# Kernel tuning notes

Hardware: AMD Instinct MI355X
Metric: run time of the kernel (lower is better)

Reference implementation:

```python
import jax, jax.numpy as jnp
import numpy as np

B, K, N, M = 32, 128, 128, 256  # batch, num_classes(==n_dim), n_dim, samples-per-matrix
EPSILON = 0.1
LAMBDA_SOFTMAX = 0.1
LEARNING_RATE = 0.01
BN_EPS = 1e-5


def setup_inputs() -> dict:
    key = jax.random.key(0)
    k1, k2, k3 = jax.random.split(key, 3)
    x = jax.random.normal(k1, (B, N, M), dtype=jnp.float32)
    A = jax.random.normal(k2, (K, N, N), dtype=jnp.float32) * 0.1
    EC_proto = jnp.einsum('kij,klj->kil', A, A)  # per-class PSD prototype covariances (K,N,N)
    EC_count = jax.random.uniform(k3, (K,), dtype=jnp.float32, minval=1.0, maxval=100.0)
    return {"x": x, "EC_proto": EC_proto, "EC_count": EC_count}


def reference(x, EC_proto, EC_count):
    n = x.shape[1]
    dtype = x.dtype
    # BatchNorm1d(num_classes, affine=False, track_running_stats=False): batch stats over (N, L)
    mean = x.mean(axis=(0, 2), keepdims=True)
    var = x.var(axis=(0, 2), keepdims=True)  # biased variance, as torch uses for normalization
    x = (x - mean) / jnp.sqrt(var + BN_EPS)

    eye = jnp.eye(n, dtype=dtype)
    total = EC_count.sum()
    has_counts = total > 1e-6

    # E branch: global expansion operator
    e_alpha = jnp.where(has_counts, n / (EPSILON * EPSILON * total), jnp.zeros((), dtype))
    e = e_alpha * jnp.linalg.inv(e_alpha * EC_proto.sum(0) + eye)  # (N,N)
    e_x_z = jnp.einsum('ij,bjm->bim', e, x)  # (B,N,M)

    # C branch: per-class compression operators
    bool_depth = (EC_count != 0).astype(dtype)  # (K,)
    count_fix = EC_count + (1.0 - bool_depth)
    c_alpha = (n / (count_fix * EPSILON * EPSILON) * bool_depth)[:, None, None]  # (K,1,1)
    c = c_alpha * jnp.linalg.inv(c_alpha * EC_proto + eye[None])  # (K,N,N)
    c_x_z = jnp.einsum('kij,bjm->bkim', c, x)  # (B,K,N,M)

    # Frobenius norm per (b,k), rescaled to sum to 10 over classes
    norm = jnp.sqrt((c_x_z * c_x_z).sum(axis=(2, 3)))  # (B,K)
    norm = 10.0 * norm / norm.sum(axis=1, keepdims=True)

    pi = jax.nn.softmax(-LAMBDA_SOFTMAX * norm, axis=1) * bool_depth  # (B,K)
    gama = jnp.where(has_counts, EC_count / total, jnp.zeros_like(EC_count))  # (K,)

    z_d = e_x_z - jnp.einsum('k,bkim,bk->bim', gama, c_x_z, pi)  # (B,N,M)
    return x + LEARNING_RATE * z_d
```

## Files before the change

### kernel.cpp

```cpp
#include <hip/hip_runtime.h>
#include <math.h>

#define Bb 32
#define Kk 128
#define Nn 128
#define Mm 256
#define EPS2 0.01f
#define LAMBDA_S 0.1f
#define LR 0.01f
#define BN_EPS_C 1e-5f

#define SWZ(c) (((c) & 14) | (((c) & 1) << 4) | (((c) >> 4) & 1))

__device__ __forceinline__ float readlane_f(float v, int lane) {
  return __int_as_float(__builtin_amdgcn_readlane(__float_as_int(v), lane));
}

__global__ void kA_bn_psum(const float* __restrict__ x, const float* __restrict__ P,
                           float* __restrict__ xn, float* __restrict__ Psum) {
  int t = threadIdx.x;
  if (blockIdx.x < 128) {
    int n = blockIdx.x;
    float v[32];
    float s = 0.f, s2 = 0.f;
    #pragma unroll
    for (int b = 0; b < Bb; ++b) {
      v[b] = x[(size_t)b * (Nn * Mm) + n * Mm + t];
      s += v[b];
      s2 += v[b] * v[b];
    }
    #pragma unroll
    for (int o = 32; o > 0; o >>= 1) {
      s += __shfl_down(s, o, 64);
      s2 += __shfl_down(s2, o, 64);
    }
    __shared__ float rs[4], rs2[4];
    if ((t & 63) == 0) { rs[t >> 6] = s; rs2[t >> 6] = s2; }
    __syncthreads();
    float S = rs[0] + rs[1] + rs[2] + rs[3];
    float S2 = rs2[0] + rs2[1] + rs2[2] + rs2[3];
    float mean = S * (1.0f / (Bb * Mm));
    float var = S2 * (1.0f / (Bb * Mm)) - mean * mean;
    float rstd = 1.0f / sqrtf(var + BN_EPS_C);
    #pragma unroll
    for (int b = 0; b < Bb; ++b)
      xn[(size_t)b * (Nn * Mm) + n * Mm + t] = (v[b] - mean) * rstd;
  } else {
    int e = (blockIdx.x - 128) * 256 + t;
    float s = 0.f;
    #pragma unroll 8
    for (int k = 0; k < Kk; ++k) s += P[(size_t)k * 16384 + e];
    Psum[e] = s;
  }
}

__global__ __launch_bounds__(256, 1) void k3S(
    const float* __restrict__ P, const float* __restrict__ Psum,
    const float* __restrict__ cnt, float* __restrict__ C,
    const float* __restrict__ xn, float* __restrict__ S) {
  __shared__ __align__(16) float LB[8448];
  int bx = blockIdx.x;
  int t = threadIdx.x;

  if (bx < 129) {
    float* Mt = LB;
    float* Rb = LB + 2112;
    float* redc = LB + 4160;
    int blk = bx;
    int tx = t & 15, ty = t >> 4;

    float cv = cnt[t & 127];
    float sr = cv;
    #pragma unroll
    for (int o = 32; o > 0; o >>= 1) sr += __shfl_down(sr, o, 64);
    if ((t & 63) == 0) redc[t >> 6] = sr;
    __syncthreads();
    float total = redc[0] + redc[1];
    bool has = total > 1e-6f;
    float av;
    if (blk < 128) {
      float c = cnt[blk];
      float bk = (c != 0.0f) ? 1.0f : 0.0f;
      float cfix = c + (1.0f - bk);
      av = (float)Nn / (cfix * EPS2) * bk;
    } else {
      av = has ? ((float)Nn / (EPS2 * total)) : 0.0f;
    }
    const float* src = (blk < 128) ? (P + (size_t)blk * 16384) : Psum;

    float a[8][8];
    #pragma unroll
    for (int i = 0; i < 8; ++i) {
      int row = ty * 8 + i;
      float4 p0 = *(const float4*)&src[row * 128 + tx * 8];
      float4 p1 = *(const float4*)&src[row * 128 + tx * 8 + 4];
      a[i][0] = av * p0.x; a[i][1] = av * p0.y; a[i][2] = av * p0.z; a[i][3] = av * p0.w;
      a[i][4] = av * p1.x; a[i][5] = av * p1.y; a[i][6] = av * p1.z; a[i][7] = av * p1.w;
      if (tx == ty) a[i][i] += 1.0f;
    }

    for (int kb = 0; kb < 8; ++kb) {
      int k0 = kb * 16;
      if ((ty >> 1) == kb) {
        int d = ty & 1;
        #pragma unroll
        for (int i = 0; i < 8; ++i) {
          *(float4*)&Rb[(d * 8 + i) * 128 + SWZ(2 * tx) * 4] =
              make_float4(a[i][0], a[i][1], a[i][2], a[i][3]);
          *(float4*)&Rb[(d * 8 + i) * 128 + SWZ(2 * tx + 1) * 4] =
              make_float4(a[i][4], a[i][5], a[i][6], a[i][7]);
        }
      }
      if ((tx >> 1) == kb) {
        int dh = tx & 1;
        #pragma unroll
        for (int i = 0; i < 8; ++i)
          #pragma unroll
          for (int j = 0; j < 8; ++j)
            Mt[(dh * 8 + j) * 132 + ty * 8 + i] = a[i][j];
      }
      __syncthreads();

      if (t < 64) {
        int l = t;
        float m[2][16];
        #pragma unroll
        for (int d = 0; d < 2; ++d)
          #pragma unroll
          for (int j = 0; j < 16; ++j)
            m[d][j] = Mt[j * 132 + 2 * l + d];
        #pragma unroll
        for (int q = 0; q < 16; ++q) {
          int lq = (k0 + q) >> 1;
          float pr[16];
          #pragma unroll
          for (int j = 0; j < 16; ++j) pr[j] = readlane_f(m[q & 1][j], lq);
          float piv = pr[q];
          float r0 = __builtin_amdgcn_rcpf(piv);
          float pinv = r0 * (2.0f - piv * r0);
          #pragma unroll
          for (int d = 0; d < 2; ++d) {
            float f = m[d][q];
            bool isp = (2 * l + d == k0 + q);
            float g = isp ? (1.0f - pinv) : f * pinv;
            #pragma unroll
            for (int j = 0; j < 16; ++j) m[d][j] = fmaf(-g, pr[j], m[d][j]);
            m[d][q] = isp ? pinv : -g;
          }
        }
        #pragma unroll
        for (int d = 0; d < 2; ++d)
          #pragma unroll
          for (int j = 0; j < 16; ++j)
            Mt[j * 132 + 2 * l + d] = m[d][j];
      }
      __syncthreads();

      if ((ty >> 1) == kb) {
        #pragma unroll
        for (int i = 0; i < 8; ++i)
          #pragma unroll
          for (int j = 0; j < 8; ++j) a[i][j] = 0.0f;
      }
      #pragma unroll
      for (int q = 0; q < 16; ++q) {
        float4 m0 = *(const float4*)&Mt[q * 132 + ty * 8];
        float4 m1 = *(const float4*)&Mt[q * 132 + ty * 8 + 4];
        float4 r0 = *(const float4*)&Rb[q * 128 + SWZ(2 * tx) * 4];
        float4 r1 = *(const float4*)&Rb[q * 128 + SWZ(2 * tx + 1) * 4];
        float mq[8] = {m0.x, m0.y, m0.z, m0.w, m1.x, m1.y, m1.z, m1.w};
        float rq[8] = {r0.x, r0.y, r0.z, r0.w, r1.x, r1.y, r1.z, r1.w};
        #pragma unroll
        for (int i = 0; i < 8; ++i)
          #pragma unroll
          for (int j = 0; j < 8; ++j)
            a[i][j] = fmaf(mq[i], rq[j], a[i][j]);
      }
      if ((tx >> 1) == kb) {
        int dh = tx & 1;
        #pragma unroll
        for (int j = 0; j < 8; ++j) {
          float4 v0 = *(const float4*)&Mt[(dh * 8 + j) * 132 + ty * 8];
          float4 v1 = *(const float4*)&Mt[(dh * 8 + j) * 132 + ty * 8 + 4];
          a[0][j] = v0.x; a[1][j] = v0.y; a[2][j] = v0.z; a[3][j] = v0.w;
          a[4][j] = v1.x; a[5][j] = v1.y; a[6][j] = v1.z; a[7][j] = v1.w;
        }
      }
      __syncthreads();
    }

    float* dst = C + (size_t)blk * 16384;
    #pragma unroll
    for (int i = 0; i < 8; ++i) {
      int row = ty * 8 + i;
      float4 v0 = make_float4(av * a[i][0], av * a[i][1], av * a[i][2], av * a[i][3]);
      float4 v1 = make_float4(av * a[i][4], av * a[i][5], av * a[i][6], av * a[i][7]);
      *(float4*)&dst[row * 128 + tx * 8] = v0;
      *(float4*)&dst[row * 128 + tx * 8 + 4] = v1;
    }
  } else {
    int bxx = bx - 129;
    int b = bxx >> 1;
    int jbase = (bxx & 1) * 64;
    float* X = LB;
    int tx = t & 15, ty = t >> 4;
    float acc[8][4] = {};
    for (int mc = 0; mc < Mm; mc += 64) {
      __syncthreads();
      for (int c = 0; c < 32; ++c) {
        int e = c * 256 + t;
        int i = e >> 6, mm = e & 63;
        X[i * 65 + mm] = xn[(size_t)b * (Nn * Mm) + i * Mm + mc + mm];
      }
      __syncthreads();
      for (int mm = 0; mm < 64; ++mm) {
        float ai[8], bj[4];
        #pragma unroll
        for (int q = 0; q < 8; ++q) ai[q] = X[(ty * 8 + q) * 65 + mm];
        #pragma unroll
        for (int q = 0; q < 4; ++q) bj[q] = X[(jbase + tx * 4 + q) * 65 + mm];
        #pragma unroll
        for (int qi = 0; qi < 8; ++qi)
          #pragma unroll
          for (int qj = 0; qj < 4; ++qj)
            acc[qi][qj] = fmaf(ai[qi], bj[qj], acc[qi][qj]);
      }
    }
    float* dst = S + (size_t)b * 16384;
    #pragma unroll
    for (int qi = 0; qi < 8; ++qi) {
      float4 v = make_float4(acc[qi][0], acc[qi][1], acc[qi][2], acc[qi][3]);
      *(float4*)&dst[(ty * 8 + qi) * 128 + jbase + tx * 4] = v;
    }
  }
}

__global__ __launch_bounds__(256, 1) void kGN(const float* __restrict__ C,
                                              const float* __restrict__ S,
                                              float* __restrict__ norm2h) {
  __shared__ __align__(16) float LB[128 * 128];
  __shared__ float redb[4][32];
  int k = blockIdx.x >> 1, h = blockIdx.x & 1;
  int t = threadIdx.x;
  const float* src = C + (size_t)k * 16384;
  for (int c = 0; c < 64; ++c) LB[c * 256 + t] = src[c * 256 + t];
  __syncthreads();
  int tx = t & 15, ty = t >> 4;
  int i0 = ty * 8, j0 = h * 64 + tx * 4;
  float acc[8][4] = {};
  for (int l = 0; l < 128; ++l) {
    float ai[8], bj[4];
    *(float4*)&ai[0] = *(const float4*)&LB[l * 128 + i0];
    *(float4*)&ai[4] = *(const float4*)&LB[l * 128 + i0 + 4];
    *(float4*)&bj[0] = *(const float4*)&LB[l * 128 + j0];
    #pragma unroll
    for (int qi = 0; qi < 8; ++qi)
      #pragma unroll
      for (int qj = 0; qj < 4; ++qj)
        acc[qi][qj] = fmaf(ai[qi], bj[qj], acc[qi][qj]);
  }
  __syncthreads();
  #pragma unroll
  for (int qi = 0; qi < 8; ++qi)
    *(float4*)&LB[(i0 + qi) * 64 + tx * 4] =
        make_float4(acc[qi][0], acc[qi][1], acc[qi][2], acc[qi][3]);
  __syncthreads();
  float nacc[32];
  #pragma unroll
  for (int b = 0; b < 32; ++b) nacc[b] = 0.0f;
  #pragma unroll
  for (int q = 0; q < 8; ++q) {
    int el = (q * 256 + t) * 4;
    float4 g = *(const float4*)&LB[el];
    int i = el >> 6, jl = el & 63;
    const float* sb = S + i * 128 + h * 64 + jl;
    #pragma unroll
    for (int b = 0; b < 32; ++b) {
      float4 sv = *(const float4*)&sb[(size_t)b * 16384];
      nacc[b] = fmaf(g.x, sv.x, nacc[b]);
      nacc[b] = fmaf(g.y, sv.y, nacc[b]);
      nacc[b] = fmaf(g.z, sv.z, nacc[b]);
      nacc[b] = fmaf(g.w, sv.w, nacc[b]);
    }
  }
  #pragma unroll
  for (int b = 0; b < 32; ++b) {
    float v = nacc[b];
    #pragma unroll
    for (int o = 32; o > 0; o >>= 1) v += __shfl_down(v, o, 64);
    nacc[b] = v;
  }
  if ((t & 63) == 0) {
    int w = t >> 6;
    #pragma unroll
    for (int b = 0; b < 32; ++b) redb[w][b] = nacc[b];
  }
  __syncthreads();
  if (t < 32)
    norm2h[(size_t)k * 64 + h * 32 + t] =
        redb[0][t] + redb[1][t] + redb[2][t] + redb[3][t];
}

__global__ void k7n(const float* __restrict__ norm2h, const float* __restrict__ cnt,
                    float* __restrict__ wT) {
  int b = blockIdx.x;
  int k = threadIdx.x;
  float n2 = norm2h[(size_t)k * 64 + b] + norm2h[(size_t)k * 64 + 32 + b];
  float norm = sqrtf(fmaxf(n2, 0.0f));
  float cv = cnt[k];
  __shared__ float r1[2], r2[2], r3[2];
  float tt = cv, r = norm;
  #pragma unroll
  for (int o = 32; o > 0; o >>= 1) {
    tt += __shfl_down(tt, o, 64);
    r += __shfl_down(r, o, 64);
  }
  if ((k & 63) == 0) { r1[k >> 6] = tt; r2[k >> 6] = r; }
  __syncthreads();
  float total = r1[0] + r1[1];
  float sumn = r2[0] + r2[1];
  float nr = 10.0f * norm / fmaxf(sumn, 1e-30f);
  float ex = expf(-LAMBDA_S * nr);
  float e2 = ex;
  #pragma unroll
  for (int o = 32; o > 0; o >>= 1) e2 += __shfl_down(e2, o, 64);
  if ((k & 63) == 0) r3[k >> 6] = e2;
  __syncthreads();
  float sume = r3[0] + r3[1];
  float bk = (cv != 0.0f) ? 1.0f : 0.0f;
  float pi = (ex / sume) * bk;
  float gama = (total > 1e-6f) ? (cv / total) : 0.0f;
  wT[k * 32 + b] = gama * pi;
}

__global__ __launch_bounds__(256, 1) void k8_k(const float* __restrict__ C,
                                               const float* __restrict__ E,
                                               const float* __restrict__ wT,
                                               float* __restrict__ F) {
  int e = blockIdx.x * 256 + threadIdx.x;
  int b0 = blockIdx.y * 8;
  float acc[8];
  float ev = E[e];
  #pragma unroll
  for (int b = 0; b < 8; ++b) acc[b] = ev;
  for (int k = 0; k < 128; ++k) {
    float cv = C[(size_t)k * 16384 + e];
    const float* wk = wT + k * 32 + b0;
    #pragma unroll
    for (int b = 0; b < 8; ++b) acc[b] = fmaf(-wk[b], cv, acc[b]);
  }
  #pragma unroll
  for (int b = 0; b < 8; ++b) F[(size_t)(b0 + b) * 16384 + e] = acc[b];
}

__global__ __launch_bounds__(256, 1) void k9_k(const float* __restrict__ F,
                                               const float* __restrict__ xn,
                                               float* __restrict__ out) {
  int bx = blockIdx.x;
  int b = bx >> 3, y = bx & 7;
  int mq = y >> 1, ih = y & 1;
  __shared__ __align__(16) float Ft[64 * 68];
  __shared__ __align__(16) float Xt[64 * 68];
  int t = threadIdx.x;
  int tx = t & 15, ty = t >> 4;
  float acc[4][4] = {};
  for (int jc = 0; jc < 128; jc += 64) {
    __syncthreads();
    #pragma unroll
    for (int q = 0; q < 4; ++q) {
      int e = q * 256 + t;
      int i = e >> 4, j4 = e & 15;
      *(float4*)&Ft[i * 68 + j4 * 4] =
          *(const float4*)&F[(size_t)b * 16384 + (ih * 64 + i) * 128 + jc + j4 * 4];
    }
    #pragma unroll
    for (int q = 0; q < 4; ++q) {
      int e = q * 256 + t;
      int jj = e >> 4, m4 = e & 15;
      *(float4*)&Xt[jj * 68 + m4 * 4] =
          *(const float4*)&xn[(size_t)b * (Nn * Mm) + (jc + jj) * Mm + mq * 64 + m4 * 4];
    }
    __syncthreads();
    for (int j4 = 0; j4 < 16; ++j4) {
      float4 fi[4], xm[4];
      #pragma unroll
      for (int r = 0; r < 4; ++r)
        fi[r] = *(const float4*)&Ft[(ty * 4 + r) * 68 + j4 * 4];
      #pragma unroll
      for (int r = 0; r < 4; ++r)
        xm[r] = *(const float4*)&Xt[(j4 * 4 + r) * 68 + tx * 4];
      #pragma unroll
      for (int qi = 0; qi < 4; ++qi) {
        #pragma unroll
        for (int qm = 0; qm < 4; ++qm) {
          float xv = ((const float*)&xm[0])[qm];
          acc[qi][qm] = fmaf(fi[qi].x, xv, acc[qi][qm]);
          xv = ((const float*)&xm[1])[qm];
          acc[qi][qm] = fmaf(fi[qi].y, xv, acc[qi][qm]);
          xv = ((const float*)&xm[2])[qm];
          acc[qi][qm] = fmaf(fi[qi].z, xv, acc[qi][qm]);
          xv = ((const float*)&xm[3])[qm];
          acc[qi][qm] = fmaf(fi[qi].w, xv, acc[qi][qm]);
        }
      }
    }
  }
  int i0 = ih * 64 + ty * 4, m0 = mq * 64 + tx * 4;
  #pragma unroll
  for (int qi = 0; qi < 4; ++qi) {
    float4 xv = *(const float4*)&xn[(size_t)b * (Nn * Mm) + (i0 + qi) * Mm + m0];
    float4 o;
    o.x = fmaf(LR, acc[qi][0], xv.x);
    o.y = fmaf(LR, acc[qi][1], xv.y);
    o.z = fmaf(LR, acc[qi][2], xv.z);
    o.w = fmaf(LR, acc[qi][3], xv.w);
    *(float4*)&out[(size_t)b * (Nn * Mm) + (i0 + qi) * Mm + m0] = o;
  }
}

extern "C" void kernel_launch(void* const* d_in, const int* in_sizes, int n_in,
                              void* d_out, int out_size, void* d_ws, size_t ws_size,
                              hipStream_t stream) {
  const float* x = (const float*)d_in[0];
  const float* P = (const float*)d_in[1];
  const float* cnt = (const float*)d_in[2];
  float* out = (float*)d_out;

  float* ws = (float*)d_ws;
  float* xn = ws;
  float* C = xn + 1048576;
  float* S = C + 2113536;
  float* norm2h = S + 524288;
  float* wT = norm2h + 8192;
  float* F = wT + 4096;
  float* Psum = F + 524288;
  size_t need_bytes = (size_t)((Psum + 16384) - ws) * sizeof(float);
  if (ws_size < need_bytes) return;

  hipLaunchKernelGGL(kA_bn_psum, dim3(192), dim3(256), 0, stream, x, P, xn, Psum);
  hipLaunchKernelGGL(k3S, dim3(193), dim3(256), 0, stream, P, Psum, cnt, C, xn, S);
  hipLaunchKernelGGL(kGN, dim3(256), dim3(256), 0, stream, C, S, norm2h);
  hipLaunchKernelGGL(k7n, dim3(32), dim3(128), 0, stream, norm2h, cnt, wT);
  hipLaunchKernelGGL(k8_k, dim3(64, 4), dim3(256), 0, stream, C,
                     C + (size_t)128 * 16384, wT, F);
  hipLaunchKernelGGL(k9_k, dim3(256), dim3(256), 0, stream, F, xn, out);
}
```

Measured before the change: 162.7 us.

## Pack two matrix inversions per 512-thread block in k3S

Doubles the k3S block size to 512 threads so each block inverts two 128x128 matrices, with each half using its own shared-memory region. The grid shrinks from 193 to 129 blocks. The Gram-matrix blocks now use 512 threads to load tiles but only 256 to compute. The aim is to fit the whole launch into one wave on the CUs and to overlap the serial pivot phases of two inversions. In exchange, each block-wide __syncthreads couples the two inversions, and the higher thread count per block may limit registers.

```diff
diff --git a/kernel.cpp b/kernel.cpp
--- a/kernel.cpp
+++ b/kernel.cpp
@@ -54,7 +54,7 @@
   }
 }
 
-__global__ __launch_bounds__(256, 1) void k3S(
+__global__ __launch_bounds__(512, 1) void k3S(
     const float* __restrict__ P, const float* __restrict__ Psum,
     const float* __restrict__ cnt, float* __restrict__ C,
     const float* __restrict__ xn, float* __restrict__ S) {
@@ -62,31 +62,35 @@
   int bx = blockIdx.x;
   int t = threadIdx.x;
 
-  if (bx < 129) {
-    float* Mt = LB;
-    float* Rb = LB + 2112;
-    float* redc = LB + 4160;
-    int blk = bx;
-    int tx = t & 15, ty = t >> 4;
-
-    float cv = cnt[t & 127];
+  if (bx < 65) {
+    int h = t >> 8;
+    int tt = t & 255;
+    float* Mt = LB + h * 4224;
+    float* Rb = Mt + 2112;
+    float* redc = Mt + 4160;
+    int mat = bx * 2 + h;
+    int tx = tt & 15, ty = tt >> 4;
+
+    float cv = cnt[tt & 127];
     float sr = cv;
     #pragma unroll
     for (int o = 32; o > 0; o >>= 1) sr += __shfl_down(sr, o, 64);
-    if ((t & 63) == 0) redc[t >> 6] = sr;
+    if ((tt & 63) == 0) redc[tt >> 6] = sr;
     __syncthreads();
     float total = redc[0] + redc[1];
     bool has = total > 1e-6f;
     float av;
-    if (blk < 128) {
-      float c = cnt[blk];
+    if (mat < 128) {
+      float c = cnt[mat];
       float bk = (c != 0.0f) ? 1.0f : 0.0f;
       float cfix = c + (1.0f - bk);
       av = (float)Nn / (cfix * EPS2) * bk;
+    } else if (mat == 128) {
+      av = has ? ((float)Nn / (EPS2 * total)) : 0.0f;
     } else {
-      av = has ? ((float)Nn / (EPS2 * total)) : 0.0f;
-    }
-    const float* src = (blk < 128) ? (P + (size_t)blk * 16384) : Psum;
+      av = 0.0f;
+    }
+    const float* src = (mat < 128) ? (P + (size_t)mat * 16384) : Psum;
 
     float a[8][8];
     #pragma unroll
@@ -121,8 +125,8 @@
       }
       __syncthreads();
 
-      if (t < 64) {
-        int l = t;
+      if (tt < 64) {
+        int l = tt;
         float m[2][16];
         #pragma unroll
         for (int d = 0; d < 2; ++d)
@@ -189,48 +193,55 @@
       __syncthreads();
     }
 
-    float* dst = C + (size_t)blk * 16384;
-    #pragma unroll
-    for (int i = 0; i < 8; ++i) {
-      int row = ty * 8 + i;
-      float4 v0 = make_float4(av * a[i][0], av * a[i][1], av * a[i][2], av * a[i][3]);
-      float4 v1 = make_float4(av * a[i][4], av * a[i][5], av * a[i][6], av * a[i][7]);
-      *(float4*)&dst[row * 128 + tx * 8] = v0;
-      *(float4*)&dst[row * 128 + tx * 8 + 4] = v1;
+    if (mat < 129) {
+      float* dst = C + (size_t)mat * 16384;
+      #pragma unroll
+      for (int i = 0; i < 8; ++i) {
+        int row = ty * 8 + i;
+        float4 v0 = make_float4(av * a[i][0], av * a[i][1], av * a[i][2], av * a[i][3]);
+        float4 v1 = make_float4(av * a[i][4], av * a[i][5], av * a[i][6], av * a[i][7]);
+        *(float4*)&dst[row * 128 + tx * 8] = v0;
+        *(float4*)&dst[row * 128 + tx * 8 + 4] = v1;
+      }
     }
   } else {
-    int bxx = bx - 129;
+    int bxx = bx - 65;
     int b = bxx >> 1;
     int jbase = (bxx & 1) * 64;
     float* X = LB;
-    int tx = t & 15, ty = t >> 4;
+    int tx = t & 15, ty = (t >> 4) & 15;
     float acc[8][4] = {};
     for (int mc = 0; mc < Mm; mc += 64) {
       __syncthreads();
-      for (int c = 0; c < 32; ++c) {
-        int e = c * 256 + t;
+      #pragma unroll
+      for (int c = 0; c < 16; ++c) {
+        int e = c * 512 + t;
         int i = e >> 6, mm = e & 63;
         X[i * 65 + mm] = xn[(size_t)b * (Nn * Mm) + i * Mm + mc + mm];
       }
       __syncthreads();
-      for (int mm = 0; mm < 64; ++mm) {
-        float ai[8], bj[4];
-        #pragma unroll
-        for (int q = 0; q < 8; ++q) ai[q] = X[(ty * 8 + q) * 65 + mm];
-        #pragma unroll
-        for (int q = 0; q < 4; ++q) bj[q] = X[(jbase + tx * 4 + q) * 65 + mm];
-        #pragma unroll
-        for (int qi = 0; qi < 8; ++qi)
-          #pragma unroll
-          for (int qj = 0; qj < 4; ++qj)
-            acc[qi][qj] = fmaf(ai[qi], bj[qj], acc[qi][qj]);
-      }
-    }
-    float* dst = S + (size_t)b * 16384;
-    #pragma unroll
-    for (int qi = 0; qi < 8; ++qi) {
-      float4 v = make_float4(acc[qi][0], acc[qi][1], acc[qi][2], acc[qi][3]);
-      *(float4*)&dst[(ty * 8 + qi) * 128 + jbase + tx * 4] = v;
+      if (t < 256) {
+        for (int mm = 0; mm < 64; ++mm) {
+          float ai[8], bj[4];
+          #pragma unroll
+          for (int q = 0; q < 8; ++q) ai[q] = X[(ty * 8 + q) * 65 + mm];
+          #pragma unroll
+          for (int q = 0; q < 4; ++q) bj[q] = X[(jbase + tx * 4 + q) * 65 + mm];
+          #pragma unroll
+          for (int qi = 0; qi < 8; ++qi)
+            #pragma unroll
+            for (int qj = 0; qj < 4; ++qj)
+              acc[qi][qj] = fmaf(ai[qi], bj[qj], acc[qi][qj]);
+        }
+      }
+    }
+    if (t < 256) {
+      float* dst = S + (size_t)b * 16384;
+      #pragma unroll
+      for (int qi = 0; qi < 8; ++qi) {
+        float4 v = make_float4(acc[qi][0], acc[qi][1], acc[qi][2], acc[qi][3]);
+        *(float4*)&dst[(ty * 8 + qi) * 128 + jbase + tx * 4] = v;
+      }
     }
   }
 }
@@ -438,7 +449,7 @@
   if (ws_size < need_bytes) return;
 
   hipLaunchKernelGGL(kA_bn_psum, dim3(192), dim3(256), 0, stream, x, P, xn, Psum);
-  hipLaunchKernelGGL(k3S, dim3(193), dim3(256), 0, stream, P, Psum, cnt, C, xn, S);
+  hipLaunchKernelGGL(k3S, dim3(129), dim3(512), 0, stream, P, Psum, cnt, C, xn, S);
   hipLaunchKernelGGL(kGN, dim3(256), dim3(256), 0, stream, C, S, norm2h);
   hipLaunchKernelGGL(k7n, dim3(32), dim3(128), 0, stream, norm2h, cnt, wT);
   hipLaunchKernelGGL(k8_k, dim3(64, 4), dim3(256), 0, stream, C,
```

Measured after the change: 193.5 us. 18.9% more time.
